# Performance work log

Hardware: AMD Instinct MI355X
Metric: run time of the kernel (lower is better)

The kernel has to match this reference:

```python
import jax, jax.numpy as jnp
import numpy as np

L, B, T, D = 4, 32, 2048, 100


def setup_inputs() -> dict:
    key = jax.random.key(0)
    k1, k2 = jax.random.split(key)
    h = jax.random.normal(k1, (L, B, T, D), dtype=jnp.float32)
    old_h = jax.random.normal(k2, (L, B, T, D), dtype=jnp.float32)
    layer_weights = jnp.ones((L,), dtype=jnp.float32)
    class_weights = jnp.ones((D,), dtype=jnp.float32)
    return {"h": h, "old_h": old_h, "layer_weights": layer_weights, "class_weights": class_weights}


def reference(h, old_h, layer_weights, class_weights):
    # h, old_h: [L, B, T, D]. Softmax / log_softmax are over the T axis
    # (dim=-1 of h[..., c] which is [B, T]).
    logq = jax.nn.log_softmax(h, axis=2)        # student log-probs  [L,B,T,D]
    logp = jax.nn.log_softmax(old_h, axis=2)    # teacher log-probs  [L,B,T,D]
    p = jnp.exp(logp)                            # teacher probs
    # KL(p || q) per (layer, class), batchmean reduction: sum over (B,T) / B
    kl_lc = jnp.sum(p * (logp - logq), axis=(1, 2)) / jnp.float32(B)  # [L, D]
    lw = jax.nn.softmax(layer_weights)           # [L]
    cw = jax.nn.softmax(class_weights)           # [D]
    loss = jnp.einsum('l,ld,d->', lw, kl_lc, cw)
    return loss
```

## Files before the change

kernel.cpp:

```cpp
#include <hip/hip_runtime.h>

constexpr int kL = 4;
constexpr int kB = 32;
constexpr int kT = 2048;
constexpr int kD = 100;
constexpr int kD4 = kD / 4;
constexpr int kCH = 16;
constexpr int kTSUB = kT / kCH;
constexpr int kLB = kL * kB;
constexpr int kROWS = kLB * kD;
constexpr int kNBLK = kLB * kCH;

#define KL_PAIR(hx, ox)                                                      \
  {                                                                          \
    const float ea = __expf(ox.x), eb = __expf(ox.y), ec = __expf(ox.z),     \
                ed = __expf(ox.w);                                           \
    sp.x += ea; sp.y += eb; sp.z += ec; sp.w += ed;                          \
    sq.x += __expf(hx.x); sq.y += __expf(hx.y);                              \
    sq.z += __expf(hx.z); sq.w += __expf(hx.w);                              \
    w.x += ea * (ox.x - hx.x); w.y += eb * (ox.y - hx.y);                    \
    w.z += ec * (ox.z - hx.z); w.w += ed * (ox.w - hx.w);                    \
  }

typedef float vfloat4 __attribute__((ext_vector_type(4)));

__device__ __forceinline__ float4 ntload4(const float4* __restrict__ p) {
  const vfloat4 v = __builtin_nontemporal_load((const vfloat4*)p);
  return make_float4(v.x, v.y, v.z, v.w);
}

__device__ __forceinline__ void stream_slab(const float4* __restrict__ hp,
                                            const float4* __restrict__ op,
                                            float4& sp, float4& sq, float4& w) {
#pragma unroll
  for (int i = 0; i < 4; ++i) {
    const float4 h0 = ntload4(hp + 0);
    const float4 h1 = ntload4(hp + 200);
    const float4 h2 = ntload4(hp + 400);
    const float4 h3 = ntload4(hp + 600);
    const float4 o0 = ntload4(op + 0);
    const float4 o1 = ntload4(op + 200);
    const float4 o2 = ntload4(op + 400);
    const float4 o3 = ntload4(op + 600);
    hp += 800; op += 800;
    __builtin_amdgcn_sched_barrier(0);
    KL_PAIR(h0, o0)
    KL_PAIR(h1, o1)
    KL_PAIR(h2, o2)
    KL_PAIR(h3, o3)
  }
}

__device__ __forceinline__ void partial_body(const float4* __restrict__ h4,
                                             const float4* __restrict__ oh4,
                                             float4& sp, float4& sq, float4& w,
                                             int lb, int chunk, int tid) {
  const int ty = tid >> 6;
  const int lane = tid & 63;
  const int half = lane / kD4;
  const int d4 = lane - half * kD4;
  const bool active = (lane < 2 * kD4);
  if (active) {
    const int row0 = chunk * kTSUB + ty * 2 + half;
    const size_t b4 = ((size_t)lb * kT + row0) * kD4 + d4;
    stream_slab(h4 + b4, oh4 + b4, sp, sq, w);
  }
}

__global__ __launch_bounds__(256) void kl_partial_na(
    const float4* __restrict__ h4, const float4* __restrict__ oh4,
    float* __restrict__ psp, float* __restrict__ psq, float* __restrict__ pw) {
  const int lb = blockIdx.x >> 4;
  const int chunk = blockIdx.x & 15;
  const int tid = threadIdx.x;

  float4 sp = {0.f, 0.f, 0.f, 0.f};
  float4 sq = {0.f, 0.f, 0.f, 0.f};
  float4 w  = {0.f, 0.f, 0.f, 0.f};
  partial_body(h4, oh4, sp, sq, w, lb, chunk, tid);

  __shared__ float red[256][12];
  {
    float* r = red[tid];
    r[0] = sp.x; r[1] = sp.y; r[2]  = sp.z; r[3]  = sp.w;
    r[4] = sq.x; r[5] = sq.y; r[6]  = sq.z; r[7]  = sq.w;
    r[8] = w.x;  r[9] = w.y;  r[10] = w.z;  r[11] = w.w;
  }
  __syncthreads();
  if (tid < kD) {
    const int dd4 = tid >> 2, j = tid & 3;
    float asp = 0.f, asq = 0.f, aw = 0.f;
#pragma unroll
    for (int g = 0; g < 4; ++g) {
#pragma unroll
      for (int hh = 0; hh < 2; ++hh) {
        const float* s = red[g * 64 + hh * kD4 + dd4];
        asp += s[j]; asq += s[4 + j]; aw += s[8 + j];
      }
    }
    const int base = blockIdx.x * kD + tid;
    psp[base] = asp;
    psq[base] = asq;
    pw[base]  = aw;
  }
}

__global__ __launch_bounds__(256) void kl_reduce_na(
    const float* __restrict__ psp, const float* __restrict__ psq,
    const float* __restrict__ pw, const float* __restrict__ lwin,
    const float* __restrict__ cwin, float* __restrict__ lbsum) {
  const int lb = blockIdx.x;
  const int tid = threadIdx.x;
  __shared__ float lwS;
  __shared__ float cw[kD];
  __shared__ float sred[256];

  if (tid == 0) {
    float m = lwin[0];
    for (int i = 1; i < kL; ++i) m = fmaxf(m, lwin[i]);
    float e[kL], s = 0.f;
    for (int i = 0; i < kL; ++i) { e[i] = __expf(lwin[i] - m); s += e[i]; }
    lwS = e[lb / kB] / s;
  }
  if (tid == 64) {
    float m = cwin[0];
    for (int i = 1; i < kD; ++i) m = fmaxf(m, cwin[i]);
    float s = 0.f;
    for (int i = 0; i < kD; ++i) { const float e = __expf(cwin[i] - m); cw[i] = e; s += e; }
    const float inv = 1.0f / s;
    for (int i = 0; i < kD; ++i) cw[i] *= inv;
  }
  __syncthreads();

  float acc = 0.f;
  if (tid < kD) {
    float asp = 0.f, asq = 0.f, aw = 0.f;
#pragma unroll
    for (int c = 0; c < kCH; ++c) {
      const int idx = (lb * kCH + c) * kD + tid;
      asp += psp[idx]; asq += psq[idx]; aw += pw[idx];
    }
    const float val = aw / asp - __logf(asp) + __logf(asq);
    acc = lwS * cw[tid] * val * (1.0f / (float)kB);
  }
  sred[tid] = acc;
  __syncthreads();
  for (int s = 128; s > 0; s >>= 1) {
    if (tid < s) sred[tid] += sred[tid + s];
    __syncthreads();
  }
  if (tid == 0) lbsum[lb] = sred[0];
}

__global__ void kl_final(const float* __restrict__ lbsum, float* __restrict__ out) {
  const int tid = threadIdx.x;
  float v = lbsum[tid] + lbsum[tid + 64];
  for (int off = 32; off > 0; off >>= 1) v += __shfl_down(v, off);
  if (tid == 0) out[0] = v;
}

__global__ __launch_bounds__(256) void kl_partial_at(
    const float4* __restrict__ h4, const float4* __restrict__ oh4,
    float* __restrict__ wsp, float* __restrict__ wsq, float* __restrict__ ww) {
  const int lb = blockIdx.x >> 4;
  const int chunk = blockIdx.x & 15;
  const int tid = threadIdx.x;

  float4 sp = {0.f, 0.f, 0.f, 0.f};
  float4 sq = {0.f, 0.f, 0.f, 0.f};
  float4 w  = {0.f, 0.f, 0.f, 0.f};
  partial_body(h4, oh4, sp, sq, w, lb, chunk, tid);

  __shared__ float red[256][12];
  {
    float* r = red[tid];
    r[0] = sp.x; r[1] = sp.y; r[2]  = sp.z; r[3]  = sp.w;
    r[4] = sq.x; r[5] = sq.y; r[6]  = sq.z; r[7]  = sq.w;
    r[8] = w.x;  r[9] = w.y;  r[10] = w.z;  r[11] = w.w;
  }
  __syncthreads();
  if (tid < kD) {
    const int dd4 = tid >> 2, j = tid & 3;
    float asp = 0.f, asq = 0.f, aw = 0.f;
#pragma unroll
    for (int g = 0; g < 4; ++g) {
#pragma unroll
      for (int hh = 0; hh < 2; ++hh) {
        const float* s = red[g * 64 + hh * kD4 + dd4];
        asp += s[j]; asq += s[4 + j]; aw += s[8 + j];
      }
    }
    const int idx = lb * kD + tid;
    atomicAdd(&wsp[idx], asp);
    atomicAdd(&wsq[idx], asq);
    atomicAdd(&ww[idx],  aw);
  }
}

__global__ __launch_bounds__(256) void kl_reduce_at(
    const float* __restrict__ wsp, const float* __restrict__ wsq,
    const float* __restrict__ ww, const float* __restrict__ lwin,
    const float* __restrict__ cwin, float* __restrict__ acc) {
  __shared__ float lw[kL];
  __shared__ float cw[kD];
  __shared__ float sred[256];
  const int tid = threadIdx.x;

  if (tid == 0) {
    float m = lwin[0];
    for (int i = 1; i < kL; ++i) m = fmaxf(m, lwin[i]);
    float e[kL], s = 0.f;
    for (int i = 0; i < kL; ++i) { e[i] = __expf(lwin[i] - m); s += e[i]; }
    const float inv = 1.0f / s;
    for (int i = 0; i < kL; ++i) lw[i] = e[i] * inv;
  }
  if (tid == 64) {
    float m = cwin[0];
    for (int i = 1; i < kD; ++i) m = fmaxf(m, cwin[i]);
    float s = 0.f;
    for (int i = 0; i < kD; ++i) { const float e = __expf(cwin[i] - m); cw[i] = e; s += e; }
    const float inv = 1.0f / s;
    for (int i = 0; i < kD; ++i) cw[i] *= inv;
  }
  __syncthreads();

  const int r = blockIdx.x * 256 + tid;
  const int l = r / (kB * kD);
  const int d = r % kD;
  const float spv = wsp[r], sqv = wsq[r], wv = ww[r];
  const float val = wv / spv - __logf(spv) + __logf(sqv);
  sred[tid] = lw[l] * cw[d] * val;
  __syncthreads();
  for (int s = 128; s > 0; s >>= 1) {
    if (tid < s) sred[tid] += sred[tid + s];
    __syncthreads();
  }
  if (tid == 0) atomicAdd(acc, sred[0]);
}

__global__ void kl_write(const float* __restrict__ acc, float* __restrict__ out) {
  out[0] = acc[0] / (float)kB;
}

extern "C" void kernel_launch(void* const* d_in, const int* in_sizes, int n_in,
                              void* d_out, int out_size, void* d_ws, size_t ws_size,
                              hipStream_t stream) {
  const float* h    = (const float*)d_in[0];
  const float* oh   = (const float*)d_in[1];
  const float* lwin = (const float*)d_in[2];
  const float* cwin = (const float*)d_in[3];

  const size_t needA = ((size_t)3 * kNBLK * kD + kLB) * sizeof(float);
  if (ws_size >= needA) {
    float* psp   = (float*)d_ws;
    float* psq   = psp + (size_t)kNBLK * kD;
    float* pw    = psq + (size_t)kNBLK * kD;
    float* lbsum = pw  + (size_t)kNBLK * kD;
    kl_partial_na<<<kNBLK, 256, 0, stream>>>(
        (const float4*)h, (const float4*)oh, psp, psq, pw);
    kl_reduce_na<<<kLB, 256, 0, stream>>>(psp, psq, pw, lwin, cwin, lbsum);
    kl_final<<<1, 64, 0, stream>>>(lbsum, (float*)d_out);
  } else {
    float* wsp = (float*)d_ws;
    float* wsq = wsp + kROWS;
    float* ww  = wsq + kROWS;
    float* acc = ww + kROWS;
    (void)hipMemsetAsync(d_ws, 0, ((size_t)3 * kROWS + 1) * sizeof(float), stream);
    kl_partial_at<<<kNBLK, 256, 0, stream>>>(
        (const float4*)h, (const float4*)oh, wsp, wsq, ww);
    kl_reduce_at<<<kROWS / 256, 256, 0, stream>>>(wsp, wsq, ww, lwin, cwin, acc);
    kl_write<<<1, 1, 0, stream>>>(acc, (float*)d_out);
  }
}
```

Before: 216.2 us.

## Stage inputs through LDS with global_load_lds in the no-atomic partial kernel

Rewrites kl_partial_na so each block copies its h and old_h slabs straight into shared memory with the direct global-to-LDS load builtin, in four stages, and then computes the KL partial sums from LDS. The previous version used non-temporal float4 register loads spread across lanes. The aim is fully dense, coalesced loads with no idle lanes during the copy. The cost is a full vmcnt wait plus two barriers per stage with no double buffering, so load latency is exposed at each step.

```diff
diff --git a/kernel.cpp b/kernel.cpp
--- a/kernel.cpp
+++ b/kernel.cpp
@@ -11,6 +11,7 @@
 constexpr int kROWS = kLB * kD;
 constexpr int kNBLK = kLB * kCH;
 
+
 #define KL_PAIR(hx, ox)                                                      \
   {                                                                          \
     const float ea = __expf(ox.x), eb = __expf(ox.y), ec = __expf(ox.z),     \
@@ -23,10 +24,139 @@
   }
 
 typedef float vfloat4 __attribute__((ext_vector_type(4)));
+typedef const __attribute__((address_space(1))) void gvoid_t;
+typedef __attribute__((address_space(3))) void lvoid_t;
 
 __device__ __forceinline__ float4 ntload4(const float4* __restrict__ p) {
   const vfloat4 v = __builtin_nontemporal_load((const vfloat4*)p);
   return make_float4(v.x, v.y, v.z, v.w);
+}
+
+__global__ __launch_bounds__(256) void kl_partial_na(
+    const float4* __restrict__ h4, const float4* __restrict__ oh4,
+    float* __restrict__ psp, float* __restrict__ psq, float* __restrict__ pw) {
+  const int lb = blockIdx.x >> 4;
+  const int chunk = blockIdx.x & 15;
+  const int tid = threadIdx.x;
+  const int ty = tid >> 6;
+  const int lane = tid & 63;
+  const int half = lane / kD4;
+  const int d4 = lane - half * kD4;
+  const bool active = (lane < 2 * kD4);
+
+  __shared__ float4 tile[1600];
+  __shared__ float red[256][12];
+
+  float4 sp = {0.f, 0.f, 0.f, 0.f};
+  float4 sq = {0.f, 0.f, 0.f, 0.f};
+  float4 w  = {0.f, 0.f, 0.f, 0.f};
+
+  const size_t blockbyte = ((size_t)lb * kT + chunk * kTSUB) * 400;
+  const char* __restrict__ hb0 = (const char*)h4 + blockbyte;
+  const char* __restrict__ ob0 = (const char*)oh4 + blockbyte;
+  char* const tl = (char*)&tile[0];
+
+  for (int s = 0; s < 4; ++s) {
+    const char* __restrict__ hb = hb0 + s * 12800;
+    const char* __restrict__ ob = ob0 + s * 12800;
+    for (int k = ty; k < 25; k += 4) {
+      const int off = k * 1024 + lane * 16;
+      const char* src = (off < 12800) ? (hb + off) : (ob + (off - 12800));
+      __builtin_amdgcn_global_load_lds((gvoid_t*)(const void*)src,
+                                       (lvoid_t*)(void*)(tl + k * 1024),
+                                       16, 0, 2 );
+    }
+    asm volatile("s_waitcnt vmcnt(0)" ::: "memory");
+    __syncthreads();
+    if (active) {
+#pragma unroll
+      for (int k2 = 0; k2 < 4; ++k2) {
+        const int r = ty * 2 + half + k2 * 8;
+        const float4 hv = tile[r * kD4 + d4];
+        const float4 ov = tile[800 + r * kD4 + d4];
+        KL_PAIR(hv, ov)
+      }
+    }
+    __syncthreads();
+  }
+
+  {
+    float* r = red[tid];
+    r[0] = sp.x; r[1] = sp.y; r[2]  = sp.z; r[3]  = sp.w;
+    r[4] = sq.x; r[5] = sq.y; r[6]  = sq.z; r[7]  = sq.w;
+    r[8] = w.x;  r[9] = w.y;  r[10] = w.z;  r[11] = w.w;
+  }
+  __syncthreads();
+  if (tid < kD) {
+    const int dd4 = tid >> 2, j = tid & 3;
+    float asp = 0.f, asq = 0.f, aw = 0.f;
+#pragma unroll
+    for (int g = 0; g < 4; ++g) {
+#pragma unroll
+      for (int hh = 0; hh < 2; ++hh) {
+        const float* sdat = red[g * 64 + hh * kD4 + dd4];
+        asp += sdat[j]; asq += sdat[4 + j]; aw += sdat[8 + j];
+      }
+    }
+    const int base = blockIdx.x * kD + tid;
+    psp[base] = asp;
+    psq[base] = asq;
+    pw[base]  = aw;
+  }
+}
+
+__global__ __launch_bounds__(256) void kl_reduce_na(
+    const float* __restrict__ psp, const float* __restrict__ psq,
+    const float* __restrict__ pw, const float* __restrict__ lwin,
+    const float* __restrict__ cwin, float* __restrict__ lbsum) {
+  const int lb = blockIdx.x;
+  const int tid = threadIdx.x;
+  __shared__ float lwS;
+  __shared__ float cw[kD];
+  __shared__ float sred[256];
+
+  if (tid == 0) {
+    float m = lwin[0];
+    for (int i = 1; i < kL; ++i) m = fmaxf(m, lwin[i]);
+    float e[kL], s = 0.f;
+    for (int i = 0; i < kL; ++i) { e[i] = __expf(lwin[i] - m); s += e[i]; }
+    lwS = e[lb / kB] / s;
+  }
+  if (tid == 64) {
+    float m = cwin[0];
+    for (int i = 1; i < kD; ++i) m = fmaxf(m, cwin[i]);
+    float s = 0.f;
+    for (int i = 0; i < kD; ++i) { const float e = __expf(cwin[i] - m); cw[i] = e; s += e; }
+    const float inv = 1.0f / s;
+    for (int i = 0; i < kD; ++i) cw[i] *= inv;
+  }
+  __syncthreads();
+
+  float acc = 0.f;
+  if (tid < kD) {
+    float asp = 0.f, asq = 0.f, aw = 0.f;
+#pragma unroll
+    for (int c = 0; c < kCH; ++c) {
+      const int idx = (lb * kCH + c) * kD + tid;
+      asp += psp[idx]; asq += psq[idx]; aw += pw[idx];
+    }
+    const float val = aw / asp - __logf(asp) + __logf(asq);
+    acc = lwS * cw[tid] * val * (1.0f / (float)kB);
+  }
+  sred[tid] = acc;
+  __syncthreads();
+  for (int s = 128; s > 0; s >>= 1) {
+    if (tid < s) sred[tid] += sred[tid + s];
+    __syncthreads();
+  }
+  if (tid == 0) lbsum[lb] = sred[0];
+}
+
+__global__ void kl_final(const float* __restrict__ lbsum, float* __restrict__ out) {
+  const int tid = threadIdx.x;
+  float v = lbsum[tid] + lbsum[tid + 64];
+  for (int off = 32; off > 0; off >>= 1) v += __shfl_down(v, off);
+  if (tid == 0) out[0] = v;
 }
 
 __device__ __forceinline__ void stream_slab(const float4* __restrict__ hp,
@@ -51,125 +181,26 @@
   }
 }
 
-__device__ __forceinline__ void partial_body(const float4* __restrict__ h4,
-                                             const float4* __restrict__ oh4,
-                                             float4& sp, float4& sq, float4& w,
-                                             int lb, int chunk, int tid) {
+__global__ __launch_bounds__(256) void kl_partial_at(
+    const float4* __restrict__ h4, const float4* __restrict__ oh4,
+    float* __restrict__ wsp, float* __restrict__ wsq, float* __restrict__ ww) {
+  const int lb = blockIdx.x >> 4;
+  const int chunk = blockIdx.x & 15;
+  const int tid = threadIdx.x;
   const int ty = tid >> 6;
   const int lane = tid & 63;
   const int half = lane / kD4;
   const int d4 = lane - half * kD4;
   const bool active = (lane < 2 * kD4);
+
+  float4 sp = {0.f, 0.f, 0.f, 0.f};
+  float4 sq = {0.f, 0.f, 0.f, 0.f};
+  float4 w  = {0.f, 0.f, 0.f, 0.f};
   if (active) {
     const int row0 = chunk * kTSUB + ty * 2 + half;
     const size_t b4 = ((size_t)lb * kT + row0) * kD4 + d4;
     stream_slab(h4 + b4, oh4 + b4, sp, sq, w);
   }
-}
-
-__global__ __launch_bounds__(256) void kl_partial_na(
-    const float4* __restrict__ h4, const float4* __restrict__ oh4,
-    float* __restrict__ psp, float* __restrict__ psq, float* __restrict__ pw) {
-  const int lb = blockIdx.x >> 4;
-  const int chunk = blockIdx.x & 15;
-  const int tid = threadIdx.x;
-
-  float4 sp = {0.f, 0.f, 0.f, 0.f};
-  float4 sq = {0.f, 0.f, 0.f, 0.f};
-  float4 w  = {0.f, 0.f, 0.f, 0.f};
-  partial_body(h4, oh4, sp, sq, w, lb, chunk, tid);
-
-  __shared__ float red[256][12];
-  {
-    float* r = red[tid];
-    r[0] = sp.x; r[1] = sp.y; r[2]  = sp.z; r[3]  = sp.w;
-    r[4] = sq.x; r[5] = sq.y; r[6]  = sq.z; r[7]  = sq.w;
-    r[8] = w.x;  r[9] = w.y;  r[10] = w.z;  r[11] = w.w;
-  }
-  __syncthreads();
-  if (tid < kD) {
-    const int dd4 = tid >> 2, j = tid & 3;
-    float asp = 0.f, asq = 0.f, aw = 0.f;
-#pragma unroll
-    for (int g = 0; g < 4; ++g) {
-#pragma unroll
-      for (int hh = 0; hh < 2; ++hh) {
-        const float* s = red[g * 64 + hh * kD4 + dd4];
-        asp += s[j]; asq += s[4 + j]; aw += s[8 + j];
-      }
-    }
-    const int base = blockIdx.x * kD + tid;
-    psp[base] = asp;
-    psq[base] = asq;
-    pw[base]  = aw;
-  }
-}
-
-__global__ __launch_bounds__(256) void kl_reduce_na(
-    const float* __restrict__ psp, const float* __restrict__ psq,
-    const float* __restrict__ pw, const float* __restrict__ lwin,
-    const float* __restrict__ cwin, float* __restrict__ lbsum) {
-  const int lb = blockIdx.x;
-  const int tid = threadIdx.x;
-  __shared__ float lwS;
-  __shared__ float cw[kD];
-  __shared__ float sred[256];
-
-  if (tid == 0) {
-    float m = lwin[0];
-    for (int i = 1; i < kL; ++i) m = fmaxf(m, lwin[i]);
-    float e[kL], s = 0.f;
-    for (int i = 0; i < kL; ++i) { e[i] = __expf(lwin[i] - m); s += e[i]; }
-    lwS = e[lb / kB] / s;
-  }
-  if (tid == 64) {
-    float m = cwin[0];
-    for (int i = 1; i < kD; ++i) m = fmaxf(m, cwin[i]);
-    float s = 0.f;
-    for (int i = 0; i < kD; ++i) { const float e = __expf(cwin[i] - m); cw[i] = e; s += e; }
-    const float inv = 1.0f / s;
-    for (int i = 0; i < kD; ++i) cw[i] *= inv;
-  }
-  __syncthreads();
-
-  float acc = 0.f;
-  if (tid < kD) {
-    float asp = 0.f, asq = 0.f, aw = 0.f;
-#pragma unroll
-    for (int c = 0; c < kCH; ++c) {
-      const int idx = (lb * kCH + c) * kD + tid;
-      asp += psp[idx]; asq += psq[idx]; aw += pw[idx];
-    }
-    const float val = aw / asp - __logf(asp) + __logf(asq);
-    acc = lwS * cw[tid] * val * (1.0f / (float)kB);
-  }
-  sred[tid] = acc;
-  __syncthreads();
-  for (int s = 128; s > 0; s >>= 1) {
-    if (tid < s) sred[tid] += sred[tid + s];
-    __syncthreads();
-  }
-  if (tid == 0) lbsum[lb] = sred[0];
-}
-
-__global__ void kl_final(const float* __restrict__ lbsum, float* __restrict__ out) {
-  const int tid = threadIdx.x;
-  float v = lbsum[tid] + lbsum[tid + 64];
-  for (int off = 32; off > 0; off >>= 1) v += __shfl_down(v, off);
-  if (tid == 0) out[0] = v;
-}
-
-__global__ __launch_bounds__(256) void kl_partial_at(
-    const float4* __restrict__ h4, const float4* __restrict__ oh4,
-    float* __restrict__ wsp, float* __restrict__ wsq, float* __restrict__ ww) {
-  const int lb = blockIdx.x >> 4;
-  const int chunk = blockIdx.x & 15;
-  const int tid = threadIdx.x;
-
-  float4 sp = {0.f, 0.f, 0.f, 0.f};
-  float4 sq = {0.f, 0.f, 0.f, 0.f};
-  float4 w  = {0.f, 0.f, 0.f, 0.f};
-  partial_body(h4, oh4, sp, sq, w, lb, chunk, tid);
 
   __shared__ float red[256][12];
   {
```

New measurement: 217.0 us. No clear change (+0.4%).
